# Kernel tuning notes

Hardware: AMD Instinct MI355X
Metric: run time of the kernel (lower is better)

## Reference

```python
import jax, jax.numpy as jnp
import numpy as np

N, E, D, C = 100000, 3200000, 256, 47


def _l2norm(x):
    n = jnp.sqrt(jnp.sum(x * x, axis=-1, keepdims=True))
    return x / jnp.maximum(n, 1e-12)


def setup_inputs() -> dict:
    key = jax.random.key(0)
    ks = jax.random.split(key, 12)
    w = lambda k, s: jax.random.normal(k, s, dtype=jnp.float32) * 0.05
    return {
        "x": jax.random.normal(ks[0], (N, D), dtype=jnp.float32),
        "src": jax.random.randint(ks[1], (E,), 0, N, dtype=jnp.int32),
        "dst": jnp.sort(jax.random.randint(ks[2], (E,), 0, N, dtype=jnp.int32)),
        "W_pre": w(ks[3], (D, D)), "b_pre": jnp.zeros((D,), jnp.float32),
        "Wl1": w(ks[4], (D, D)), "bl1": jnp.zeros((D,), jnp.float32),
        "Wr1": w(ks[5], (D, D)),
        "Wl2": w(ks[6], (D, D)), "bl2": jnp.zeros((D,), jnp.float32),
        "Wr2": w(ks[7], (D, D)),
        "W_jk": w(ks[8], (D, D)), "b_jk": jnp.zeros((D,), jnp.float32),
        "W_post": w(ks[9], (C, D)), "b_post": jnp.zeros((C,), jnp.float32),
    }


def _sage_conv(x, src, dst, Wl, bl, Wr):
    # aggr='add': m_i = sum_{j in N(i)} x_j  (SpMM as gather + segment_sum)
    m = jax.ops.segment_sum(x[src], dst, num_segments=N)
    out = m @ Wl.T + bl + x @ Wr.T  # lin_l(aggr) + lin_r(root)
    return _l2norm(out)            # SAGEConv normalize=True


def reference(x, src, dst, W_pre, b_pre, Wl1, bl1, Wr1, Wl2, bl2, Wr2,
              W_jk, b_jk, W_post, b_post):
    # pre-MLP (1 layer) + classifier activation; dropout=0, batch_norm off
    h = jax.nn.relu(x @ W_pre.T + b_pre)
    h = _l2norm(h)  # self.normalize
    # GraphSAGE, jk='last': act+dropout after every conv, then jk lin
    h = jax.nn.relu(_sage_conv(h, src, dst, Wl1, bl1, Wr1))
    h = jax.nn.relu(_sage_conv(h, src, dst, Wl2, bl2, Wr2))
    h = h @ W_jk.T + b_jk
    # post: act + post-MLP (1 layer)
    h = jax.nn.relu(h)
    h = h @ W_post.T + b_post
    return jax.nn.log_softmax(h, axis=-1)
```

## Files before the change

### kernel.cpp

```cpp
#include <hip/hip_runtime.h>
#include <stdint.h>

#define DEV __device__ __forceinline__

typedef __attribute__((ext_vector_type(8))) short bh8;
typedef __attribute__((ext_vector_type(4))) float f4;
#define LDS_AS __attribute__((address_space(3)))
#define GLB_AS __attribute__((address_space(1)))

DEV unsigned short f2bf(float f) {
    union { float f; uint32_t u; } c; c.f = f;
    uint32_t u = c.u;
    uint32_t r = (u + 0x7fffu + ((u >> 16) & 1u)) >> 16;
    return (unsigned short)r;
}
DEV float bf2f(unsigned short h) {
    union { uint32_t u; float f; } c; c.u = ((uint32_t)h) << 16;
    return c.f;
}

DEV uint8_t f2fp8(float v) {
    const float vs = v * 256.f;
    union { float f; uint32_t u; } c; c.f = vs;
    const uint32_t u = c.u + 0x7ffffu + ((c.u >> 20) & 1u);
    const uint32_t f8 = (u >> 20) - 960u;
    return (vs < 0.015625f) ? (uint8_t)0 : (uint8_t)f8;
}
DEV float fp8w(uint32_t x) { union { uint32_t u; float f; } c; c.u = x; return c.f; }

DEV void gload16(const void* g, void* l) {
    __builtin_amdgcn_global_load_lds((const GLB_AS uint32_t*)g, (LDS_AS uint32_t*)l, 16, 0, 0);
}

__global__ __launch_bounds__(256) void prep_kernel(
    const float* __restrict__ x, unsigned short* __restrict__ xb, int n4x, int nbx,
    const float* __restrict__ w0, const float* __restrict__ w1, const float* __restrict__ w2,
    const float* __restrict__ w3, const float* __restrict__ w4, const float* __restrict__ w5,
    unsigned short* __restrict__ wbBase,
    const int* __restrict__ dst, int* __restrict__ rp, int N, int E) {
    const int b = blockIdx.x;
    if (b < nbx) {
        const int i = b * 256 + threadIdx.x;
        if (i < n4x) {
            const float4 v = ((const float4*)x)[i];
            ushort4 o; o.x = f2bf(v.x); o.y = f2bf(v.y); o.z = f2bf(v.z); o.w = f2bf(v.w);
            ((ushort4*)xb)[i] = o;
        }
    } else if (b < nbx + 384) {
        const int wi = (b - nbx) >> 6;
        const int i = ((b - nbx) & 63) * 256 + threadIdx.x;
        const float* s = wi == 0 ? w0 : wi == 1 ? w1 : wi == 2 ? w2 : wi == 3 ? w3 : wi == 4 ? w4 : w5;
        const float4 v = ((const float4*)s)[i];
        ushort4 o; o.x = f2bf(v.x); o.y = f2bf(v.y); o.z = f2bf(v.z); o.w = f2bf(v.w);
        ((ushort4*)(wbBase + (size_t)wi * 65536))[i] = o;
    } else {
        const int i = (b - nbx - 384) * 256 + threadIdx.x;
        if (i <= N) {
            int lo = 0, hi = E;
            while (lo < hi) { int mid = (lo + hi) >> 1; if (dst[mid] < i) lo = mid + 1; else hi = mid; }
            rp[i] = lo;
        }
    }
}

__global__ __launch_bounds__(256) void agg_fp8_kernel(const uint32_t* __restrict__ h32,
                                                      const int* __restrict__ src,
                                                      const int* __restrict__ rp,
                                                      unsigned short* __restrict__ mout, int nNodes) {
    const int node = blockIdx.x * 4 + (threadIdx.x >> 6);
    if (node >= nNodes) return;
    const int lane = threadIdx.x & 63;
    const int beg = __builtin_amdgcn_readfirstlane(rp[node]);
    const int end = __builtin_amdgcn_readfirstlane(rp[node + 1]);
    float a0 = 0.f, a1 = 0.f, a2 = 0.f, a3 = 0.f;
    int e = beg;
    for (; e + 8 <= end; e += 8) {
        int s[8];
#pragma unroll
        for (int i = 0; i < 8; i++) s[i] = src[e + i];
        uint32_t w[8];
#pragma unroll
        for (int i = 0; i < 8; i++) w[i] = h32[(size_t)s[i] * 64 + lane];
#pragma unroll
        for (int i = 0; i < 8; i++) {
            a0 += fp8w((w[i] << 20) & 0x07f00000u);
            a1 += fp8w((w[i] << 12) & 0x07f00000u);
            a2 += fp8w((w[i] << 4)  & 0x07f00000u);
            a3 += fp8w((w[i] >> 4)  & 0x07f00000u);
        }
    }
    for (; e < end; ++e) {
        const uint32_t w = h32[(size_t)src[e] * 64 + lane];
        a0 += fp8w((w << 20) & 0x07f00000u);
        a1 += fp8w((w << 12) & 0x07f00000u);
        a2 += fp8w((w << 4)  & 0x07f00000u);
        a3 += fp8w((w >> 4)  & 0x07f00000u);
    }
    const float sc = 0x1p112f;
    ushort4 o;
    o.x = f2bf(a0 * sc); o.y = f2bf(a1 * sc); o.z = f2bf(a2 * sc); o.w = f2bf(a3 * sc);
    *(ushort4*)&mout[(size_t)node * 256 + (size_t)lane * 4] = o;
}

__global__ __launch_bounds__(256) void agg_kernel(const unsigned short* __restrict__ h,
                                                  const int* __restrict__ src,
                                                  const int* __restrict__ rp,
                                                  unsigned short* __restrict__ mout, int nNodes) {
    const int node = blockIdx.x * 4 + (threadIdx.x >> 6);
    if (node >= nNodes) return;
    const int lane = threadIdx.x & 63;
    const size_t fo = (size_t)lane * 4;
    const int beg = __builtin_amdgcn_readfirstlane(rp[node]);
    const int end = __builtin_amdgcn_readfirstlane(rp[node + 1]);
    float a0 = 0.f, a1 = 0.f, a2 = 0.f, a3 = 0.f;
    int e = beg;
    for (; e + 4 <= end; e += 4) {
        const int s0 = src[e], s1 = src[e+1], s2 = src[e+2], s3 = src[e+3];
        ushort4 v0 = *(const ushort4*)&h[(size_t)s0 * 256 + fo];
        ushort4 v1 = *(const ushort4*)&h[(size_t)s1 * 256 + fo];
        ushort4 v2 = *(const ushort4*)&h[(size_t)s2 * 256 + fo];
        ushort4 v3 = *(const ushort4*)&h[(size_t)s3 * 256 + fo];
        a0 += bf2f(v0.x) + bf2f(v1.x) + bf2f(v2.x) + bf2f(v3.x);
        a1 += bf2f(v0.y) + bf2f(v1.y) + bf2f(v2.y) + bf2f(v3.y);
        a2 += bf2f(v0.z) + bf2f(v1.z) + bf2f(v2.z) + bf2f(v3.z);
        a3 += bf2f(v0.w) + bf2f(v1.w) + bf2f(v2.w) + bf2f(v3.w);
    }
    for (; e < end; ++e) {
        const int s = src[e];
        ushort4 v = *(const ushort4*)&h[(size_t)s * 256 + fo];
        a0 += bf2f(v.x); a1 += bf2f(v.y); a2 += bf2f(v.z); a3 += bf2f(v.w);
    }
    ushort4 o;
    o.x = f2bf(a0); o.y = f2bf(a1); o.z = f2bf(a2); o.w = f2bf(a3);
    *(ushort4*)&mout[(size_t)node * 256 + fo] = o;
}

template <int NSEG, int EPMODE, bool EMIT>
__global__ __launch_bounds__(512) void gemm_kernel(
    const unsigned short* __restrict__ A0, const unsigned short* __restrict__ A1,
    const unsigned short* __restrict__ B0, const unsigned short* __restrict__ B1,
    const float* __restrict__ bias, unsigned short* __restrict__ Out,
    uint8_t* __restrict__ F8, int M) {
    __shared__ unsigned short Alds[128 * 32];
    __shared__ unsigned short Blds[256 * 32];
    __shared__ float ssq_lds[8][64];

    const int t = threadIdx.x;
    const int wid = t >> 6;
    const int lane = t & 63;
    const int wr = wid >> 2, wc = wid & 3;
    const int l15 = lane & 15;
    const int kh = lane >> 4;
    const int rowBase = blockIdx.x * 128;

    f4 acc[4][4];
#pragma unroll
    for (int m = 0; m < 4; m++)
#pragma unroll
        for (int n = 0; n < 4; n++) acc[m][n] = f4{0.f, 0.f, 0.f, 0.f};

    const int rA = t >> 2;
    const int sSlotA = (t & 3) ^ ((rA >> 1) & 3);
    int grA = rowBase + rA; if (grA > M - 1) grA = M - 1;
    const size_t gAoff = (size_t)grA * 256 + sSlotA * 8;
    const size_t gBoff0 = (size_t)rA * 256 + sSlotA * 8;
    const size_t gBoff1 = (size_t)(128 + rA) * 256 + sSlotA * 8;
    unsigned short* AldsW = &Alds[wid * 512];
    unsigned short* BldsW0 = &Blds[wid * 512];
    unsigned short* BldsW1 = &Blds[4096 + wid * 512];

#pragma unroll
    for (int seg = 0; seg < NSEG; ++seg) {
        const unsigned short* Ap = (NSEG == 2 && seg == 1) ? A1 : A0;
        const unsigned short* Bp = (NSEG == 2 && seg == 1) ? B1 : B0;
        for (int k0 = 0; k0 < 256; k0 += 32) {
            __syncthreads();
            gload16(Ap + gAoff + k0, AldsW);
            gload16(Bp + gBoff0 + k0, BldsW0);
            gload16(Bp + gBoff1 + k0, BldsW1);
            __syncthreads();
            bh8 a[4], b[4];
#pragma unroll
            for (int m = 0; m < 4; m++) {
                const int ra = wr * 64 + m * 16 + l15;
                a[m] = *(const bh8*)&Alds[ra * 32 + ((kh ^ ((ra >> 1) & 3)) * 8)];
            }
#pragma unroll
            for (int n = 0; n < 4; n++) {
                const int rb = wc * 64 + n * 16 + l15;
                b[n] = *(const bh8*)&Blds[rb * 32 + ((kh ^ ((rb >> 1) & 3)) * 8)];
            }
#pragma unroll
            for (int m = 0; m < 4; m++)
#pragma unroll
                for (int n = 0; n < 4; n++)
                    acc[m][n] = __builtin_amdgcn_mfma_f32_16x16x32_bf16(a[m], b[n], acc[m][n], 0, 0, 0);
        }
    }

    const int cBase = wc * 64 + l15;
    float sq[4][4];
#pragma unroll
    for (int m = 0; m < 4; m++) { sq[m][0] = 0.f; sq[m][1] = 0.f; sq[m][2] = 0.f; sq[m][3] = 0.f; }
#pragma unroll
    for (int n = 0; n < 4; n++) {
        const float bv = bias[cBase + n * 16];
#pragma unroll
        for (int m = 0; m < 4; m++)
#pragma unroll
            for (int r = 0; r < 4; r++) {
                float v = acc[m][n][r] + bv;
                if (EPMODE != 1) v = fmaxf(v, 0.f);
                acc[m][n][r] = v;
                sq[m][r] += v * v;
            }
    }

    if (EPMODE != 2) {
#pragma unroll
        for (int mask = 1; mask < 16; mask <<= 1)
#pragma unroll
            for (int m = 0; m < 4; m++)
#pragma unroll
                for (int r = 0; r < 4; r++) sq[m][r] += __shfl_xor(sq[m][r], mask);
        if (l15 == 0) {
#pragma unroll
            for (int m = 0; m < 4; m++)
#pragma unroll
                for (int r = 0; r < 4; r++) ssq_lds[wid][m * 16 + kh * 4 + r] = sq[m][r];
        }
        __syncthreads();
#pragma unroll
        for (int m = 0; m < 4; m++)
#pragma unroll
            for (int r = 0; r < 4; r++) {
                const int rr = m * 16 + kh * 4 + r;
                const float s = ssq_lds[wr * 4 + 0][rr] + ssq_lds[wr * 4 + 1][rr] +
                                ssq_lds[wr * 4 + 2][rr] + ssq_lds[wr * 4 + 3][rr];
                sq[m][r] = 1.f / fmaxf(sqrtf(s), 1e-12f);
            }
    }

#pragma unroll
    for (int m = 0; m < 4; m++)
#pragma unroll
        for (int r = 0; r < 4; r++) {
            const int grow = rowBase + wr * 64 + m * 16 + kh * 4 + r;
            if (grow < M) {
#pragma unroll
                for (int n = 0; n < 4; n++) {
                    float v = acc[m][n][r];
                    if (EPMODE != 2) v *= sq[m][r];
                    if (EPMODE == 1) v = fmaxf(v, 0.f);
                    Out[(size_t)grow * 256 + cBase + n * 16] = f2bf(v);
                    if (EMIT) F8[(size_t)grow * 256 + cBase + n * 16] = f2fp8(v);
                }
            }
        }
}

__global__ __launch_bounds__(256) void final_kernel(const unsigned short* __restrict__ T,
                                                    const float* __restrict__ Wp,
                                                    const float* __restrict__ bp,
                                                    float* __restrict__ out, int M) {
    __shared__ unsigned short Wlds[48 * 256];
    const int t = threadIdx.x;
    for (int i = t; i < 48 * 32; i += 256) {
        const int rb = i >> 5, slot = i & 31;
        bh8 o;
        if (rb < 47) {
#pragma unroll
            for (int j = 0; j < 8; j++) o[j] = (short)f2bf(Wp[rb * 256 + slot * 8 + j]);
        } else {
#pragma unroll
            for (int j = 0; j < 8; j++) o[j] = 0;
        }
        *(bh8*)&Wlds[rb * 256 + ((slot ^ (rb & 7)) * 8)] = o;
    }
    __syncthreads();
    const int wave = t >> 6, lane = t & 63;
    const int l15 = lane & 15, kh = lane >> 4;
    const int rowBase = blockIdx.x * 64 + wave * 16;
    int gr = rowBase + l15; if (gr > M - 1) gr = M - 1;

    bh8 a[8];
#pragma unroll
    for (int ks = 0; ks < 8; ks++)
        a[ks] = *(const bh8*)&T[(size_t)gr * 256 + ks * 32 + kh * 8];
    f4 acc[3];
#pragma unroll
    for (int n = 0; n < 3; n++) acc[n] = f4{0.f, 0.f, 0.f, 0.f};
#pragma unroll
    for (int ks = 0; ks < 8; ks++)
#pragma unroll
        for (int n = 0; n < 3; n++) {
            const int rb = n * 16 + l15;
            const bh8 b = *(const bh8*)&Wlds[rb * 256 + (((ks * 4 + kh) ^ (rb & 7)) * 8)];
            acc[n] = __builtin_amdgcn_mfma_f32_16x16x32_bf16(a[ks], b, acc[n], 0, 0, 0);
        }

    const int c0 = l15, c1 = 16 + l15, c2 = 32 + l15;
    const float b0 = bp[c0], b1 = bp[c1];
    const float b2 = (l15 < 15) ? bp[c2] : 0.f;
#pragma unroll
    for (int r = 0; r < 4; r++) {
        const int grow = rowBase + kh * 4 + r;
        const float x0 = acc[0][r] + b0;
        const float x1 = acc[1][r] + b1;
        const float x2 = (l15 < 15) ? (acc[2][r] + b2) : -3.0e38f;
        float mx = fmaxf(fmaxf(x0, x1), x2);
#pragma unroll
        for (int msk = 1; msk < 16; msk <<= 1) mx = fmaxf(mx, __shfl_xor(mx, msk));
        float se = __expf(x0 - mx) + __expf(x1 - mx) + ((l15 < 15) ? __expf(x2 - mx) : 0.f);
#pragma unroll
        for (int msk = 1; msk < 16; msk <<= 1) se += __shfl_xor(se, msk);
        const float ls = __logf(se) + mx;
        if (grow < M) {
            float* orow = &out[(size_t)grow * 47];
            orow[c0] = x0 - ls;
            orow[c1] = x1 - ls;
            if (l15 < 15) orow[c2] = x2 - ls;
        }
    }
}

extern "C" void kernel_launch(void* const* d_in, const int* in_sizes, int n_in,
                              void* d_out, int out_size, void* d_ws, size_t ws_size,
                              hipStream_t stream) {
    const float* x      = (const float*)d_in[0];
    const int*   src    = (const int*)d_in[1];
    const int*   dst    = (const int*)d_in[2];
    const float* W_pre  = (const float*)d_in[3];
    const float* b_pre  = (const float*)d_in[4];
    const float* Wl1    = (const float*)d_in[5];
    const float* bl1    = (const float*)d_in[6];
    const float* Wr1    = (const float*)d_in[7];
    const float* Wl2    = (const float*)d_in[8];
    const float* bl2    = (const float*)d_in[9];
    const float* Wr2    = (const float*)d_in[10];
    const float* W_jk   = (const float*)d_in[11];
    const float* b_jk   = (const float*)d_in[12];
    const float* W_post = (const float*)d_in[13];
    const float* b_post = (const float*)d_in[14];

    const int N = in_sizes[0] / 256;
    const int E = in_sizes[1];

    char* ws = (char*)d_ws;
    char* ws0 = ws;
    const size_t HB = (size_t)N * 256 * 2;
    unsigned short* bufA = (unsigned short*)ws; ws += HB;
    unsigned short* bufB = (unsigned short*)ws; ws += HB;
    unsigned short* bufC = (unsigned short*)ws; ws += HB;
    unsigned short* bufD = (unsigned short*)ws; ws += HB;
    unsigned short* wbBase = (unsigned short*)ws; ws += (size_t)6 * 65536 * 2;
    int* rp = (int*)ws; ws += (size_t)(N + 1) * 4;
    uint8_t* f8 = (uint8_t*)ws; ws += (size_t)N * 256;
    const bool useFp8 = ((size_t)(ws - ws0) <= ws_size);

    const int n4x = (N * 256) / 4;
    const int nbx = (n4x + 255) / 256;
    const int nbr = (N + 1 + 255) / 256;
    prep_kernel<<<nbx + 384 + nbr, 256, 0, stream>>>(x, bufA, n4x, nbx,
        W_pre, Wl1, Wr1, Wl2, Wr2, W_jk, wbBase, dst, rp, N, E);
    unsigned short* wb[6];
    for (int i = 0; i < 6; i++) wb[i] = wbBase + (size_t)i * 65536;

    const int gB = (N + 127) / 128;
    const int gAgg = (N + 3) / 4;
    if (useFp8) {
        gemm_kernel<1, 0, true><<<gB, 512, 0, stream>>>(bufA, nullptr, wb[0], nullptr, b_pre, bufB, f8, N);
        agg_fp8_kernel<<<gAgg, 256, 0, stream>>>((const uint32_t*)f8, src, rp, bufC, N);
        gemm_kernel<2, 1, true><<<gB, 512, 0, stream>>>(bufC, bufB, wb[1], wb[2], bl1, bufD, f8, N);
        agg_fp8_kernel<<<gAgg, 256, 0, stream>>>((const uint32_t*)f8, src, rp, bufC, N);
        gemm_kernel<2, 1, false><<<gB, 512, 0, stream>>>(bufC, bufD, wb[3], wb[4], bl2, bufA, nullptr, N);
        gemm_kernel<1, 2, false><<<gB, 512, 0, stream>>>(bufA, nullptr, wb[5], nullptr, b_jk, bufB, nullptr, N);
    } else {
        gemm_kernel<1, 0, false><<<gB, 512, 0, stream>>>(bufA, nullptr, wb[0], nullptr, b_pre, bufB, nullptr, N);
        agg_kernel<<<gAgg, 256, 0, stream>>>(bufB, src, rp, bufC, N);
        gemm_kernel<2, 1, false><<<gB, 512, 0, stream>>>(bufC, bufB, wb[1], wb[2], bl1, bufD, nullptr, N);
        agg_kernel<<<gAgg, 256, 0, stream>>>(bufD, src, rp, bufC, N);
        gemm_kernel<2, 1, false><<<gB, 512, 0, stream>>>(bufC, bufD, wb[3], wb[4], bl2, bufA, nullptr, N);
        gemm_kernel<1, 2, false><<<gB, 512, 0, stream>>>(bufA, nullptr, wb[5], nullptr, b_jk, bufB, nullptr, N);
    }
    final_kernel<<<(N + 63) / 64, 256, 0, stream>>>(bufB, W_post, b_post, (float*)d_out, N);
}
```

Baseline: 611.1 us.

## Split FP8 aggregation across feature chunks with edge-parallel lanes and shuffle reduction

Each node's 256-feature aggregation is split across 8 blocks, each covering a 32-byte feature chunk. Within a wavefront, 8 lanes cover the chunk's dwords and 8 lane groups process different edges in parallel, followed by an xor-shuffle reduction. The aim is more memory parallelism and more blocks for low-degree nodes. In exchange, the src indices and row pointers are re-read by 8 blocks per node, each gather is only 32 bytes, and a shuffle reduction is added.

```diff
diff --git a/kernel.cpp b/kernel.cpp
--- a/kernel.cpp
+++ b/kernel.cpp
@@ -67,39 +67,49 @@
                                                       const int* __restrict__ src,
                                                       const int* __restrict__ rp,
                                                       unsigned short* __restrict__ mout, int nNodes) {
-    const int node = blockIdx.x * 4 + (threadIdx.x >> 6);
+    const int chunk = blockIdx.x & 7;
+    const int node = (blockIdx.x >> 3) * 4 + (threadIdx.x >> 6);
     if (node >= nNodes) return;
     const int lane = threadIdx.x & 63;
+    const int dw = lane & 7;
+    const int es = lane >> 3;
+    const int cbase = chunk * 8 + dw;
     const int beg = __builtin_amdgcn_readfirstlane(rp[node]);
     const int end = __builtin_amdgcn_readfirstlane(rp[node + 1]);
     float a0 = 0.f, a1 = 0.f, a2 = 0.f, a3 = 0.f;
     int e = beg;
-    for (; e + 8 <= end; e += 8) {
-        int s[8];
-#pragma unroll
-        for (int i = 0; i < 8; i++) s[i] = src[e + i];
-        uint32_t w[8];
-#pragma unroll
-        for (int i = 0; i < 8; i++) w[i] = h32[(size_t)s[i] * 64 + lane];
-#pragma unroll
-        for (int i = 0; i < 8; i++) {
-            a0 += fp8w((w[i] << 20) & 0x07f00000u);
-            a1 += fp8w((w[i] << 12) & 0x07f00000u);
-            a2 += fp8w((w[i] << 4)  & 0x07f00000u);
-            a3 += fp8w((w[i] >> 4)  & 0x07f00000u);
-        }
-    }
-    for (; e < end; ++e) {
-        const uint32_t w = h32[(size_t)src[e] * 64 + lane];
+    for (; e + 16 <= end; e += 16) {
+        const int sA = src[e + es];
+        const int sB = src[e + 8 + es];
+        const uint32_t wA = h32[(size_t)sA * 64 + cbase];
+        const uint32_t wB = h32[(size_t)sB * 64 + cbase];
+        a0 += fp8w((wA << 20) & 0x07f00000u) + fp8w((wB << 20) & 0x07f00000u);
+        a1 += fp8w((wA << 12) & 0x07f00000u) + fp8w((wB << 12) & 0x07f00000u);
+        a2 += fp8w((wA << 4)  & 0x07f00000u) + fp8w((wB << 4)  & 0x07f00000u);
+        a3 += fp8w((wA >> 4)  & 0x07f00000u) + fp8w((wB >> 4)  & 0x07f00000u);
+    }
+    for (; e < end; e += 8) {
+        const int ee = e + es;
+        const int sv = src[(ee < end) ? ee : (end - 1)];
+        const uint32_t w = (ee < end) ? h32[(size_t)sv * 64 + cbase] : 0u;
         a0 += fp8w((w << 20) & 0x07f00000u);
         a1 += fp8w((w << 12) & 0x07f00000u);
         a2 += fp8w((w << 4)  & 0x07f00000u);
         a3 += fp8w((w >> 4)  & 0x07f00000u);
     }
-    const float sc = 0x1p112f;
-    ushort4 o;
-    o.x = f2bf(a0 * sc); o.y = f2bf(a1 * sc); o.z = f2bf(a2 * sc); o.w = f2bf(a3 * sc);
-    *(ushort4*)&mout[(size_t)node * 256 + (size_t)lane * 4] = o;
+#pragma unroll
+    for (int mask = 8; mask < 64; mask <<= 1) {
+        a0 += __shfl_xor(a0, mask);
+        a1 += __shfl_xor(a1, mask);
+        a2 += __shfl_xor(a2, mask);
+        a3 += __shfl_xor(a3, mask);
+    }
+    if (es == 0) {
+        const float sc = 0x1p112f;
+        ushort4 o;
+        o.x = f2bf(a0 * sc); o.y = f2bf(a1 * sc); o.z = f2bf(a2 * sc); o.w = f2bf(a3 * sc);
+        *(ushort4*)&mout[(size_t)node * 256 + chunk * 32 + dw * 4] = o;
+    }
 }
 
 __global__ __launch_bounds__(256) void agg_kernel(const unsigned short* __restrict__ h,
@@ -370,9 +380,9 @@
     const int gAgg = (N + 3) / 4;
     if (useFp8) {
         gemm_kernel<1, 0, true><<<gB, 512, 0, stream>>>(bufA, nullptr, wb[0], nullptr, b_pre, bufB, f8, N);
-        agg_fp8_kernel<<<gAgg, 256, 0, stream>>>((const uint32_t*)f8, src, rp, bufC, N);
+        agg_fp8_kernel<<<8 * gAgg, 256, 0, stream>>>((const uint32_t*)f8, src, rp, bufC, N);
         gemm_kernel<2, 1, true><<<gB, 512, 0, stream>>>(bufC, bufB, wb[1], wb[2], bl1, bufD, f8, N);
-        agg_fp8_kernel<<<gAgg, 256, 0, stream>>>((const uint32_t*)f8, src, rp, bufC, N);
+        agg_fp8_kernel<<<8 * gAgg, 256, 0, stream>>>((const uint32_t*)f8, src, rp, bufC, N);
         gemm_kernel<2, 1, false><<<gB, 512, 0, stream>>>(bufC, bufD, wb[3], wb[4], bl2, bufA, nullptr, N);
         gemm_kernel<1, 2, false><<<gB, 512, 0, stream>>>(bufA, nullptr, wb[5], nullptr, b_jk, bufB, nullptr, N);
     } else {
```

Measured after the change: 1.417 ms. +131.9%, slower.

## Double-buffer LDS tiles in GEMM kernel to overlap global loads with MFMA

Applied to the files above, without the earlier changes.

Doubles the A and B shared-memory tiles and restructures the K loop into a single flattened stage loop. The next stage's global-to-LDS loads are issued before the current stage's MFMAs, so each step needs one barrier instead of two. This is meant to hide global load latency behind compute, at the cost of twice the LDS per block, which may lower occupancy.

```diff
diff --git a/kernel.cpp b/kernel.cpp
--- a/kernel.cpp
+++ b/kernel.cpp
@@ -141,8 +141,8 @@
     const unsigned short* __restrict__ B0, const unsigned short* __restrict__ B1,
     const float* __restrict__ bias, unsigned short* __restrict__ Out,
     uint8_t* __restrict__ F8, int M) {
-    __shared__ unsigned short Alds[128 * 32];
-    __shared__ unsigned short Blds[256 * 32];
+    __shared__ unsigned short Alds[2 * 128 * 32];
+    __shared__ unsigned short Blds[2 * 256 * 32];
     __shared__ float ssq_lds[8][64];
 
     const int t = threadIdx.x;
@@ -165,37 +165,43 @@
     const size_t gAoff = (size_t)grA * 256 + sSlotA * 8;
     const size_t gBoff0 = (size_t)rA * 256 + sSlotA * 8;
     const size_t gBoff1 = (size_t)(128 + rA) * 256 + sSlotA * 8;
-    unsigned short* AldsW = &Alds[wid * 512];
-    unsigned short* BldsW0 = &Blds[wid * 512];
-    unsigned short* BldsW1 = &Blds[4096 + wid * 512];
-
-#pragma unroll
-    for (int seg = 0; seg < NSEG; ++seg) {
-        const unsigned short* Ap = (NSEG == 2 && seg == 1) ? A1 : A0;
-        const unsigned short* Bp = (NSEG == 2 && seg == 1) ? B1 : B0;
-        for (int k0 = 0; k0 < 256; k0 += 32) {
-            __syncthreads();
-            gload16(Ap + gAoff + k0, AldsW);
-            gload16(Bp + gBoff0 + k0, BldsW0);
-            gload16(Bp + gBoff1 + k0, BldsW1);
-            __syncthreads();
-            bh8 a[4], b[4];
-#pragma unroll
-            for (int m = 0; m < 4; m++) {
-                const int ra = wr * 64 + m * 16 + l15;
-                a[m] = *(const bh8*)&Alds[ra * 32 + ((kh ^ ((ra >> 1) & 3)) * 8)];
-            }
-#pragma unroll
-            for (int n = 0; n < 4; n++) {
-                const int rb = wc * 64 + n * 16 + l15;
-                b[n] = *(const bh8*)&Blds[rb * 32 + ((kh ^ ((rb >> 1) & 3)) * 8)];
-            }
-#pragma unroll
-            for (int m = 0; m < 4; m++)
-#pragma unroll
-                for (int n = 0; n < 4; n++)
-                    acc[m][n] = __builtin_amdgcn_mfma_f32_16x16x32_bf16(a[m], b[n], acc[m][n], 0, 0, 0);
-        }
+
+    const int nsteps = NSEG * 8;
+    auto STAGE = [&](int s, int buf) {
+        const unsigned short* Ap = (NSEG == 2 && s >= 8) ? A1 : A0;
+        const unsigned short* Bp = (NSEG == 2 && s >= 8) ? B1 : B0;
+        const int k0 = (s & 7) * 32;
+        gload16(Ap + gAoff + k0, &Alds[buf * 4096 + wid * 512]);
+        gload16(Bp + gBoff0 + k0, &Blds[buf * 8192 + wid * 512]);
+        gload16(Bp + gBoff1 + k0, &Blds[buf * 8192 + 4096 + wid * 512]);
+    };
+
+    STAGE(0, 0);
+    asm volatile("s_waitcnt vmcnt(0)" ::: "memory");
+    __syncthreads();
+
+#pragma unroll 2
+    for (int s = 0; s < nsteps; ++s) {
+        const int cur = s & 1;
+        if (s + 1 < nsteps) STAGE(s + 1, cur ^ 1);
+        bh8 a[4], b[4];
+#pragma unroll
+        for (int m = 0; m < 4; m++) {
+            const int ra = wr * 64 + m * 16 + l15;
+            a[m] = *(const bh8*)&Alds[cur * 4096 + ra * 32 + ((kh ^ ((ra >> 1) & 3)) * 8)];
+        }
+#pragma unroll
+        for (int n = 0; n < 4; n++) {
+            const int rb = wc * 64 + n * 16 + l15;
+            b[n] = *(const bh8*)&Blds[cur * 8192 + rb * 32 + ((kh ^ ((rb >> 1) & 3)) * 8)];
+        }
+#pragma unroll
+        for (int m = 0; m < 4; m++)
+#pragma unroll
+            for (int n = 0; n < 4; n++)
+                acc[m][n] = __builtin_amdgcn_mfma_f32_16x16x32_bf16(a[m], b[n], acc[m][n], 0, 0, 0);
+        asm volatile("s_waitcnt vmcnt(0)" ::: "memory");
+        __syncthreads();
     }
 
     const int cBase = wc * 64 + l15;
```

After: 602.2 us. Within noise of the previous version (-1.5%).
